# Kernel tuning notes

Measured on AMD Instinct MI355X. Metric: run time of the kernel, lower is better.

Reference implementation:

```python
import jax, jax.numpy as jnp
import numpy as np

MAX_ITERATIONS = 10
TOLERANCE = 1e-4


def setup_inputs() -> dict:
    key = jax.random.key(0)
    k1, k2 = jax.random.split(key)
    B, N = 4, 2048
    p1 = jax.random.normal(k1, (B, N, 3), dtype=jnp.float32)
    p2 = jax.random.normal(k2, (B, N, 3), dtype=jnp.float32)
    return {"p1": p1, "p2": p2}


def _get_transform(p1, p2):
    # SVD-based rigid (Kabsch) transform between matched sets p1 -> p2.
    p1c = p1.mean(-2, keepdims=True)   # [B,1,3]
    p2c = p2.mean(-2, keepdims=True)   # [B,1,3]
    q1 = p1 - p1c
    q2 = p2 - p2c
    H = jnp.einsum('bnj,bnk->bjk', q2, q1)          # p2^T @ p1, [B,3,3]
    u, s, vT = jnp.linalg.svd(H)
    v = jnp.swapaxes(vT, -1, -2)
    uT = jnp.swapaxes(u, -1, -2)
    d = jnp.linalg.det(v @ uT)                      # [B], reflection fix
    v = v.at[:, 2, 2].multiply(d)
    RT = u @ jnp.swapaxes(v, -1, -2)
    R = jnp.swapaxes(RT, -1, -2)                    # [B,3,3]
    t = p2c - p1c @ R                               # [B,1,3]
    return R, t


def _nearest_neighbor(p1, p2):
    # dist[b, j, i] = ||p2[b,j] - p1[b,i]||  (matches torch broadcast layout)
    dif = p2[:, :, None, :] - p1[:, None, :, :]     # [B,N2,N1,3]
    dist = jnp.sqrt(jnp.sum(dif * dif, axis=-1))    # [B,N2,N1]
    idx = jnp.argmin(dist, axis=-1)                 # [B,N2] (topk k=1, smallest)
    vals = jnp.take_along_axis(dist, idx[..., None], axis=-1)[..., 0]
    return vals, idx


def reference(p1, p2):
    def cond(state):
        temp_pc, it, prev_err, done = state
        return (it <= MAX_ITERATIONS) & jnp.logical_not(done)

    def body(state):
        temp_pc, it, prev_err, _ = state
        vals, idx = _nearest_neighbor(temp_pc, p2)
        mean_err = vals.mean()
        # Source indexes ori_p2 with the LAST batch's indices (nn.indices[-1])
        matched = p2[:, idx[-1], :]                 # [B,N,3]
        R, t = _get_transform(temp_pc, matched)
        new_pc = temp_pc @ R + t
        done = jnp.abs(prev_err - mean_err) < TOLERANCE
        return (new_pc, it + 1, mean_err, done)

    init = (p1, jnp.int32(0), jnp.float32(0.0), jnp.bool_(False))
    temp_pc, _, _, _ = jax.lax.while_loop(cond, body, init)

    R, t = _get_transform(p1, temp_pc)
    T = jnp.concatenate([R, jnp.swapaxes(t, 1, 2)], axis=2)  # [B,3,4]
    return T
```

## Files before the change

kernel.cpp:

```cpp
#include <hip/hip_runtime.h>

#define B 4
#define N 2048
#define MAXIT 11
#define TOL 1e-4f
#define CC 64
#define QPT 4
#define QC (256*QPT)


__device__ double det3(const double* M) {
    return M[0]*(M[4]*M[8]-M[5]*M[7])
         - M[1]*(M[3]*M[8]-M[5]*M[6])
         + M[2]*(M[3]*M[7]-M[4]*M[6]);
}

__device__ void svd3x3(const double* A, double* U, double* V, double* sig) {
    double S[9];
    for (int i = 0; i < 3; ++i)
        for (int j = 0; j < 3; ++j) {
            double s = 0.0;
            for (int k = 0; k < 3; ++k) s += A[k*3+i] * A[k*3+j];
            S[i*3+j] = s;
        }
    double Vm[9] = {1,0,0, 0,1,0, 0,0,1};
    for (int sweep = 0; sweep < 30; ++sweep) {
        double off = fabs(S[1]) + fabs(S[2]) + fabs(S[5]);
        double base = fabs(S[0]) + fabs(S[4]) + fabs(S[8]);
        if (off <= 1e-15 * base) break;
        for (int pi = 0; pi < 3; ++pi) {
            const int p = (pi == 2) ? 1 : 0;
            const int q = (pi == 0) ? 1 : 2;
            double apq = S[p*3+q];
            if (apq == 0.0) continue;
            double app = S[p*3+p], aqq = S[q*3+q];
            double tau = (aqq - app) / (2.0 * apq);
            double tt  = ((tau >= 0.0) ? 1.0 : -1.0) / (fabs(tau) + sqrt(1.0 + tau*tau));
            double c = 1.0 / sqrt(1.0 + tt*tt);
            double s = tt * c;
            for (int k = 0; k < 3; ++k) {
                double skp = S[k*3+p], skq = S[k*3+q];
                S[k*3+p] = c*skp - s*skq;
                S[k*3+q] = s*skp + c*skq;
            }
            for (int k = 0; k < 3; ++k) {
                double spk = S[p*3+k], sqk = S[q*3+k];
                S[p*3+k] = c*spk - s*sqk;
                S[q*3+k] = s*spk + c*sqk;
            }
            for (int k = 0; k < 3; ++k) {
                double vkp = Vm[k*3+p], vkq = Vm[k*3+q];
                Vm[k*3+p] = c*vkp - s*vkq;
                Vm[k*3+q] = s*vkp + c*vkq;
            }
        }
    }
    double lam[3] = {S[0], S[4], S[8]};
    int ord[3] = {0, 1, 2};
    for (int i = 0; i < 2; ++i)
        for (int j = i+1; j < 3; ++j)
            if (lam[ord[j]] > lam[ord[i]]) { int tmp = ord[i]; ord[i] = ord[j]; ord[j] = tmp; }
    for (int i = 0; i < 3; ++i) {
        int o = ord[i];
        double l = lam[o] > 0.0 ? lam[o] : 0.0;
        sig[i] = sqrt(l);
        for (int k = 0; k < 3; ++k) V[k*3+i] = Vm[k*3+o];
    }
    for (int i = 0; i < 3; ++i) {
        double u0 = 0, u1 = 0, u2 = 0;
        for (int k = 0; k < 3; ++k) {
            u0 += A[0*3+k] * V[k*3+i];
            u1 += A[1*3+k] * V[k*3+i];
            u2 += A[2*3+k] * V[k*3+i];
        }
        double nrm = sqrt(u0*u0 + u1*u1 + u2*u2);
        if (nrm > 1e-300) { u0 /= nrm; u1 /= nrm; u2 /= nrm; }
        else {
            double ax = U[0], ay = U[3], az = U[6];
            double bx = U[1], by = U[4], bz = U[7];
            u0 = ay*bz - az*by; u1 = az*bx - ax*bz; u2 = ax*by - ay*bx;
        }
        U[0*3+i] = u0; U[1*3+i] = u1; U[2*3+i] = u2;
    }
}

__device__ void compute_Rt(const double* H, const double* p1c, const double* p2c,
                           float* Rout, float* tout) {
    double U[9], V[9], sig[3];
    svd3x3(H, U, V, sig);
    double d = (det3(U) * det3(V) < 0.0) ? -1.0 : 1.0;
    V[2*3+2] *= d;
    double R[9];
    for (int i = 0; i < 3; ++i)
        for (int j = 0; j < 3; ++j) {
            double s = 0.0;
            for (int k = 0; k < 3; ++k) s += V[i*3+k] * U[j*3+k];
            R[i*3+j] = s;
        }
    for (int j = 0; j < 3; ++j) {
        double s = 0.0;
        for (int k = 0; k < 3; ++k) s += p1c[k] * R[k*3+j];
        tout[j] = (float)(p2c[j] - s);
    }
    for (int k = 0; k < 9; ++k) Rout[k] = (float)R[k];
}

__device__ inline float wred(float v) {
    v += __shfl_down(v, 32);
    v += __shfl_down(v, 16);
    v += __shfl_down(v, 8);
    v += __shfl_down(v, 4);
    v += __shfl_down(v, 2);
    v += __shfl_down(v, 1);
    return v;
}

__global__ void __launch_bounds__(256) k_init(const float* __restrict__ p1,
                                              float* __restrict__ temp,
                                              unsigned long long* __restrict__ nn0,
                                              float* scal, int* done) {
    int i = blockIdx.x * blockDim.x + threadIdx.x;
    if (i < B*N*3) temp[i] = p1[i];
    if (i < B*N)   nn0[i] = ~0ULL;
    if (i == 0)    scal[0] = 0.0f;
    if (i < 12)    done[i] = 0;
}

__global__ void __launch_bounds__(256) k_nn(const float* __restrict__ p2,
                                            const float* __restrict__ temp,
                                            unsigned long long* __restrict__ nn,
                                            const int* __restrict__ done) {
    if (*done) return;
    __shared__ float4 sc4[CC];
    const int b  = blockIdx.z;
    const int qb = blockIdx.y * QC;
    const int cb = blockIdx.x * CC;
    for (int j = threadIdx.x; j < CC; j += 256) {
        const float* cp = &temp[(b*N + cb + j)*3];
        const float cx = cp[0], cy = cp[1], cz = cp[2];
        sc4[j] = make_float4(cx, cy, cz, 0.5f*(cx*cx + cy*cy + cz*cz));
    }
    __syncthreads();

    float px[QPT], py[QPT], pz[QPT], pn[QPT];
    float best[QPT];
    int   bi[QPT];
    #pragma unroll
    for (int k = 0; k < QPT; ++k) {
        const int q = qb + threadIdx.x + 256*k;
        px[k] = p2[(b*N+q)*3+0];
        py[k] = p2[(b*N+q)*3+1];
        pz[k] = p2[(b*N+q)*3+2];
        pn[k] = px[k]*px[k] + py[k]*py[k] + pz[k]*pz[k];
        best[k] = __uint_as_float(0x7f7fffffu);
        bi[k] = 0;
    }
    #pragma unroll 4
    for (int j = 0; j < CC; ++j) {
        const float4 c = sc4[j];
        #pragma unroll
        for (int k = 0; k < QPT; ++k) {
            float s = __builtin_fmaf(-px[k], c.x,
                      __builtin_fmaf(-py[k], c.y,
                      __builtin_fmaf(-pz[k], c.z, c.w)));
            if (s < best[k]) { best[k] = s; bi[k] = cb + j; }
        }
    }
    #pragma unroll
    for (int k = 0; k < QPT; ++k) {
        const int q = qb + threadIdx.x + 256*k;
        float d2 = fmaxf(__builtin_fmaf(2.0f, best[k], pn[k]), 0.0f);
        unsigned long long pack =
            ((unsigned long long)__float_as_uint(d2) << 32) | (unsigned int)bi[k];
        atomicMin(&nn[b*N + q], pack);
    }
}

__global__ void __launch_bounds__(256) k_step(const float* __restrict__ p2,
                                              float* __restrict__ temp,
                                              const unsigned long long* __restrict__ nn_cur,
                                              unsigned long long* __restrict__ nn_next,
                                              float* scal,
                                              const int* __restrict__ done_cur,
                                              int* done_next) {
    const int t   = threadIdx.x;
    const int bid = blockIdx.x;
    if (*done_cur) {
        if (bid == 4 && t == 0) *done_next = 1;
        return;
    }

    if (bid == 4) {
        __shared__ float lds4[4];
        float s = 0.f;
        for (int i = t; i < B*N; i += 256) {
            unsigned int dbits = (unsigned int)(nn_cur[i] >> 32);
            s += sqrtf(__uint_as_float(dbits));
            nn_next[i] = ~0ULL;
        }
        s = wred(s);
        if ((t & 63) == 0) lds4[t >> 6] = s;
        __syncthreads();
        if (t == 0) {
            float tot = lds4[0] + lds4[1] + lds4[2] + lds4[3];
            float meanerr = tot / (float)(B*N);
            float prev = scal[0];
            scal[0] = meanerr;
            *done_next = (fabsf(prev - meanerr) < TOL) ? 1 : 0;
        }
        return;
    }

    const int b = bid;
    __shared__ float lred[4][9];
    __shared__ float sc1[3], sc2[3], sR[9], sT[3];
    const int wave = t >> 6, lane = t & 63;

    float v6[6] = {0,0,0,0,0,0};
    for (int i = t; i < N; i += 256) {
        const float* tp = &temp[(b*N + i)*3];
        v6[0] += tp[0]; v6[1] += tp[1]; v6[2] += tp[2];
        const int mi = (int)(unsigned int)(nn_cur[3*N + i] & 0xffffffffULL);
        const float* mp = &p2[(b*N + mi)*3];
        v6[3] += mp[0]; v6[4] += mp[1]; v6[5] += mp[2];
    }
    #pragma unroll
    for (int k = 0; k < 6; ++k) v6[k] = wred(v6[k]);
    if (lane == 0) {
        #pragma unroll
        for (int k = 0; k < 6; ++k) lred[wave][k] = v6[k];
    }
    __syncthreads();
    if (t == 0) {
        #pragma unroll
        for (int k = 0; k < 3; ++k) {
            sc1[k] = (lred[0][k]  +lred[1][k]  +lred[2][k]  +lred[3][k])   / (float)N;
            sc2[k] = (lred[0][3+k]+lred[1][3+k]+lred[2][3+k]+lred[3][3+k]) / (float)N;
        }
    }
    __syncthreads();
    const float c1x = sc1[0], c1y = sc1[1], c1z = sc1[2];
    const float c2x = sc2[0], c2y = sc2[1], c2z = sc2[2];

    float h[9];
    #pragma unroll
    for (int k = 0; k < 9; ++k) h[k] = 0.f;
    for (int i = t; i < N; i += 256) {
        const float* tp = &temp[(b*N + i)*3];
        const int mi = (int)(unsigned int)(nn_cur[3*N + i] & 0xffffffffULL);
        const float* mp = &p2[(b*N + mi)*3];
        const float bx = tp[0]-c1x, by = tp[1]-c1y, bz = tp[2]-c1z;
        const float ax = mp[0]-c2x, ay = mp[1]-c2y, az = mp[2]-c2z;
        h[0] += ax*bx; h[1] += ax*by; h[2] += ax*bz;
        h[3] += ay*bx; h[4] += ay*by; h[5] += ay*bz;
        h[6] += az*bx; h[7] += az*by; h[8] += az*bz;
    }
    #pragma unroll
    for (int k = 0; k < 9; ++k) h[k] = wred(h[k]);
    if (lane == 0) {
        #pragma unroll
        for (int k = 0; k < 9; ++k) lred[wave][k] = h[k];
    }
    __syncthreads();
    if (t == 0) {
        double H[9], c1d[3], c2d[3];
        for (int k = 0; k < 9; ++k)
            H[k] = (double)(lred[0][k]+lred[1][k]+lred[2][k]+lred[3][k]);
        c1d[0] = c1x; c1d[1] = c1y; c1d[2] = c1z;
        c2d[0] = c2x; c2d[1] = c2y; c2d[2] = c2z;
        compute_Rt(H, c1d, c2d, sR, sT);
    }
    __syncthreads();
    for (int i = t; i < N; i += 256) {
        float* tp = &temp[(b*N + i)*3];
        const float x = tp[0], y = tp[1], z = tp[2];
        tp[0] = x*sR[0] + y*sR[3] + z*sR[6] + sT[0];
        tp[1] = x*sR[1] + y*sR[4] + z*sR[7] + sT[1];
        tp[2] = x*sR[2] + y*sR[5] + z*sR[8] + sT[2];
    }
}

__global__ void __launch_bounds__(256) k_final(const float* __restrict__ p1,
                                               const float* __restrict__ temp,
                                               float* __restrict__ out) {
    const int b = blockIdx.x;
    const int t = threadIdx.x;
    __shared__ float lred[4][9];
    __shared__ float sc1[3], sc2[3], sR[9], sT[3];
    const int wave = t >> 6, lane = t & 63;

    float v6[6] = {0,0,0,0,0,0};
    for (int i = t; i < N; i += 256) {
        const float* pp = &p1[(b*N + i)*3];
        const float* tp = &temp[(b*N + i)*3];
        v6[0] += pp[0]; v6[1] += pp[1]; v6[2] += pp[2];
        v6[3] += tp[0]; v6[4] += tp[1]; v6[5] += tp[2];
    }
    #pragma unroll
    for (int k = 0; k < 6; ++k) v6[k] = wred(v6[k]);
    if (lane == 0) {
        #pragma unroll
        for (int k = 0; k < 6; ++k) lred[wave][k] = v6[k];
    }
    __syncthreads();
    if (t == 0) {
        #pragma unroll
        for (int k = 0; k < 3; ++k) {
            sc1[k] = (lred[0][k]  +lred[1][k]  +lred[2][k]  +lred[3][k])   / (float)N;
            sc2[k] = (lred[0][3+k]+lred[1][3+k]+lred[2][3+k]+lred[3][3+k]) / (float)N;
        }
    }
    __syncthreads();
    const float c1x = sc1[0], c1y = sc1[1], c1z = sc1[2];
    const float c2x = sc2[0], c2y = sc2[1], c2z = sc2[2];

    float h[9];
    #pragma unroll
    for (int k = 0; k < 9; ++k) h[k] = 0.f;
    for (int i = t; i < N; i += 256) {
        const float* pp = &p1[(b*N + i)*3];
        const float* tp = &temp[(b*N + i)*3];
        const float bx = pp[0]-c1x, by = pp[1]-c1y, bz = pp[2]-c1z;
        const float ax = tp[0]-c2x, ay = tp[1]-c2y, az = tp[2]-c2z;
        h[0] += ax*bx; h[1] += ax*by; h[2] += ax*bz;
        h[3] += ay*bx; h[4] += ay*by; h[5] += ay*bz;
        h[6] += az*bx; h[7] += az*by; h[8] += az*bz;
    }
    #pragma unroll
    for (int k = 0; k < 9; ++k) h[k] = wred(h[k]);
    if (lane == 0) {
        #pragma unroll
        for (int k = 0; k < 9; ++k) lred[wave][k] = h[k];
    }
    __syncthreads();
    if (t == 0) {
        double H[9], c1d[3], c2d[3];
        for (int k = 0; k < 9; ++k)
            H[k] = (double)(lred[0][k]+lred[1][k]+lred[2][k]+lred[3][k]);
        c1d[0] = c1x; c1d[1] = c1y; c1d[2] = c1z;
        c2d[0] = c2x; c2d[1] = c2y; c2d[2] = c2z;
        compute_Rt(H, c1d, c2d, sR, sT);
        for (int i = 0; i < 3; ++i) {
            out[b*12 + i*4 + 0] = sR[i*3+0];
            out[b*12 + i*4 + 1] = sR[i*3+1];
            out[b*12 + i*4 + 2] = sR[i*3+2];
            out[b*12 + i*4 + 3] = sT[i];
        }
    }
}

extern "C" void kernel_launch(void* const* d_in, const int* in_sizes, int n_in,
                              void* d_out, int out_size, void* d_ws, size_t ws_size,
                              hipStream_t stream) {
    const float* p1 = (const float*)d_in[0];
    const float* p2 = (const float*)d_in[1];
    float* out  = (float*)d_out;
    float* temp = (float*)d_ws;
    unsigned long long* nn0 = (unsigned long long*)((char*)d_ws + 98304);
    unsigned long long* nn1 = (unsigned long long*)((char*)d_ws + 163840);
    float* scal = (float*)((char*)d_ws + 229376);
    int*   done = (int*)((char*)d_ws + 229380);

    k_init<<<(B*N*3 + 255)/256, 256, 0, stream>>>(p1, temp, nn0, scal, done);
    dim3 g(N/CC, N/QC, B);
    for (int it = 0; it < MAXIT; ++it) {
        unsigned long long* nn_cur  = (it & 1) ? nn1 : nn0;
        unsigned long long* nn_next = (it & 1) ? nn0 : nn1;
        k_nn<<<g, 256, 0, stream>>>(p2, temp, nn_cur, &done[it]);
        k_step<<<5, 256, 0, stream>>>(p2, temp, nn_cur, nn_next, scal,
                                      &done[it], &done[it+1]);
    }
    k_final<<<4, 256, 0, stream>>>(p1, temp, out);
}
```

Measured before the change: 309.6 us.

## Fuse ICP loop into one cooperative persistent kernel with grid syncs

Replaces the roughly two dozen per-iteration kernel launches (init, NN, step, final) with one cooperative kernel of 256 blocks that uses grid.sync between phases. The transform is applied lazily to the staged points, and H is built from raw sums minus the N·c2·c1 centroid term, so one pass of per-block partial sums replaces the serial 4-block reductions. The NN buffer alternates between atomicMin and atomicMax on the complement, so it never needs a reset pass. It removes launch overhead and the serial single-block step kernels, but adds grid-wide barriers and slightly changes numerics by forming H from raw moments.

```diff
diff --git a/kernel.cpp b/kernel.cpp
--- a/kernel.cpp
+++ b/kernel.cpp
@@ -1,12 +1,18 @@
 #include <hip/hip_runtime.h>
+#include <hip/hip_cooperative_groups.h>
+
+namespace cg = cooperative_groups;
 
 #define B 4
 #define N 2048
 #define MAXIT 11
 #define TOL 1e-4f
+#define NBLK 256
+#define BT 256
 #define CC 64
 #define QPT 4
-#define QC (256*QPT)
+#define QC (BT*QPT)
+#define RPB 32
 
 
 __device__ double det3(const double* M) {
@@ -115,236 +121,235 @@
     return v;
 }
 
-__global__ void __launch_bounds__(256) k_init(const float* __restrict__ p1,
-                                              float* __restrict__ temp,
-                                              unsigned long long* __restrict__ nn0,
-                                              float* scal, int* done) {
-    int i = blockIdx.x * blockDim.x + threadIdx.x;
-    if (i < B*N*3) temp[i] = p1[i];
-    if (i < B*N)   nn0[i] = ~0ULL;
-    if (i == 0)    scal[0] = 0.0f;
-    if (i < 12)    done[i] = 0;
-}
-
-__global__ void __launch_bounds__(256) k_nn(const float* __restrict__ p2,
-                                            const float* __restrict__ temp,
-                                            unsigned long long* __restrict__ nn,
-                                            const int* __restrict__ done) {
-    if (*done) return;
+__device__ __forceinline__ void tf_pt(const float* __restrict__ R, const float* __restrict__ T,
+                                      float x, float y, float z,
+                                      float& ox, float& oy, float& oz) {
+    ox = x*R[0] + y*R[3] + z*R[6] + T[0];
+    oy = x*R[1] + y*R[4] + z*R[7] + T[1];
+    oz = x*R[2] + y*R[5] + z*R[8] + T[2];
+}
+
+__global__ void __launch_bounds__(BT, 1)
+icp_fused(const float* __restrict__ p1, const float* __restrict__ p2,
+          float* __restrict__ out, float* __restrict__ buf,
+          unsigned long long* __restrict__ nn,
+          float* __restrict__ part, float* __restrict__ p1s) {
+    cg::grid_group grid = cg::this_grid();
+    const int bid = blockIdx.x, tid = threadIdx.x;
+    const int b = bid >> 6, blk = bid & 63;
+    const int r0 = bid * RPB;
+    const int lane = tid & 63, wave = tid >> 6;
+
     __shared__ float4 sc4[CC];
-    const int b  = blockIdx.z;
-    const int qb = blockIdx.y * QC;
-    const int cb = blockIdx.x * CC;
-    for (int j = threadIdx.x; j < CC; j += 256) {
-        const float* cp = &temp[(b*N + cb + j)*3];
-        const float cx = cp[0], cy = cp[1], cz = cp[2];
-        sc4[j] = make_float4(cx, cy, cz, 0.5f*(cx*cx + cy*cy + cz*cz));
-    }
-    __syncthreads();
-
-    float px[QPT], py[QPT], pz[QPT], pn[QPT];
-    float best[QPT];
-    int   bi[QPT];
-    #pragma unroll
-    for (int k = 0; k < QPT; ++k) {
-        const int q = qb + threadIdx.x + 256*k;
-        px[k] = p2[(b*N+q)*3+0];
-        py[k] = p2[(b*N+q)*3+1];
-        pz[k] = p2[(b*N+q)*3+2];
-        pn[k] = px[k]*px[k] + py[k]*py[k] + pz[k]*pz[k];
-        best[k] = __uint_as_float(0x7f7fffffu);
-        bi[k] = 0;
-    }
-    #pragma unroll 4
-    for (int j = 0; j < CC; ++j) {
-        const float4 c = sc4[j];
+    __shared__ float sR[9], sT[3];
+    __shared__ float lred[4][3];
+    __shared__ int sCtl;
+
+    for (int j = tid; j < RPB*3; j += BT) buf[r0*3 + j] = p1[r0*3 + j];
+    if (tid < RPB) nn[r0 + tid] = ~0ULL;
+    if (blk == 0) {
+        float sx = 0.f, sy = 0.f, sz = 0.f;
+        for (int i = tid; i < N; i += BT) {
+            const float* pp = &p1[(b*N + i)*3];
+            sx += pp[0]; sy += pp[1]; sz += pp[2];
+        }
+        sx = wred(sx); sy = wred(sy); sz = wred(sz);
+        if (lane == 0) { lred[wave][0]=sx; lred[wave][1]=sy; lred[wave][2]=sz; }
+        __syncthreads();
+        if (tid == 0) {
+            p1s[b*3+0] = lred[0][0]+lred[1][0]+lred[2][0]+lred[3][0];
+            p1s[b*3+1] = lred[0][1]+lred[1][1]+lred[2][1]+lred[3][1];
+            p1s[b*3+2] = lred[0][2]+lred[1][2]+lred[2][2]+lred[3][2];
+        }
+    }
+    grid.sync();
+
+    int itex = MAXIT;
+    for (int it = 0; it <= MAXIT; ++it) {
+        if (it == 0) {
+            if (tid == 0) {
+                sR[0]=1.f; sR[1]=0.f; sR[2]=0.f;
+                sR[3]=0.f; sR[4]=1.f; sR[5]=0.f;
+                sR[6]=0.f; sR[7]=0.f; sR[8]=1.f;
+                sT[0]=0.f; sT[1]=0.f; sT[2]=0.f;
+                sCtl = 0;
+            }
+        } else if (wave == 0) {
+            const int slot  = (it-1) & 3;
+            const int slot2 = (it-2) & 3;
+            float a[16];
+            const float* pb = &part[((slot*B + b)*64 + lane)*16];
+            #pragma unroll
+            for (int k = 0; k < 16; ++k) a[k] = pb[k];
+            #pragma unroll
+            for (int k = 0; k < 16; ++k) a[k] = wred(a[k]);
+            float ec = 0.f;
+            #pragma unroll
+            for (int bb = 0; bb < B; ++bb)
+                ec += part[((slot*B + bb)*64 + lane)*16 + 15];
+            ec = wred(ec);
+            float ep = 0.f;
+            if (it >= 2) {
+                #pragma unroll
+                for (int bb = 0; bb < B; ++bb)
+                    ep += part[((slot2*B + bb)*64 + lane)*16 + 15];
+                ep = wred(ep);
+            }
+            if (lane == 0) {
+                const float errcur  = ec / (float)(B*N);
+                const float errprev = (it >= 2) ? ep / (float)(B*N) : 0.0f;
+                const int done = (fabsf(errprev - errcur) < TOL) ? 1 : 0;
+                double H[9], c1d[3], c2d[3];
+                c2d[0] = (double)a[0]/N; c2d[1] = (double)a[1]/N; c2d[2] = (double)a[2]/N;
+                c1d[0] = (double)a[3]/N; c1d[1] = (double)a[4]/N; c1d[2] = (double)a[5]/N;
+                for (int j = 0; j < 3; ++j)
+                    for (int k = 0; k < 3; ++k)
+                        H[j*3+k] = (double)a[6 + j*3 + k] - (double)N * c2d[j] * c1d[k];
+                compute_Rt(H, c1d, c2d, sR, sT);
+                sCtl = (done || it == MAXIT) ? 1 : 0;
+            }
+        }
+        __syncthreads();
+        if (sCtl) { itex = it; break; }
+
+        {
+            const int cb = (blk >> 1) * CC;
+            const int qb = (blk & 1) * QC;
+            if (tid < CC) {
+                const float* cp = &buf[(b*N + cb + tid)*3];
+                float cx, cy, cz;
+                tf_pt(sR, sT, cp[0], cp[1], cp[2], cx, cy, cz);
+                sc4[tid] = make_float4(cx, cy, cz, 0.5f*(cx*cx + cy*cy + cz*cz));
+            }
+            __syncthreads();
+            float px[QPT], py[QPT], pz[QPT];
+            float best[QPT];
+            int   bi[QPT];
+            #pragma unroll
+            for (int k = 0; k < QPT; ++k) {
+                const int q = qb + tid + BT*k;
+                px[k] = p2[(b*N + q)*3 + 0];
+                py[k] = p2[(b*N + q)*3 + 1];
+                pz[k] = p2[(b*N + q)*3 + 2];
+                best[k] = __uint_as_float(0x7f7fffffu);
+                bi[k] = 0;
+            }
+            #pragma unroll 4
+            for (int j = 0; j < CC; ++j) {
+                const float4 c = sc4[j];
+                #pragma unroll
+                for (int k = 0; k < QPT; ++k) {
+                    float s = __builtin_fmaf(-px[k], c.x,
+                              __builtin_fmaf(-py[k], c.y,
+                              __builtin_fmaf(-pz[k], c.z, c.w)));
+                    if (s < best[k]) { best[k] = s; bi[k] = cb + j; }
+                }
+            }
+            #pragma unroll
+            for (int k = 0; k < QPT; ++k) {
+                const int q = qb + tid + BT*k;
+                const float pn = px[k]*px[k] + py[k]*py[k] + pz[k]*pz[k];
+                float d2 = fmaxf(__builtin_fmaf(2.0f, best[k], pn), 0.0f);
+                unsigned long long K =
+                    ((unsigned long long)__float_as_uint(d2) << 32) | (unsigned int)bi[k];
+                if (it & 1) atomicMax(&nn[b*N + q], ~K);
+                else        atomicMin(&nn[b*N + q],  K);
+            }
+        }
+        grid.sync();
+
+        {
+            const int slotW = it & 3;
+            float pv[16];
+            #pragma unroll
+            for (int k = 0; k < 16; ++k) pv[k] = 0.f;
+            if (tid < RPB) {
+                const int r = r0 + tid;
+                const int i = r & (N-1);
+                unsigned long long pk = nn[r];
+                if (it & 1) pk = ~pk;
+                const unsigned int dbits = (unsigned int)(pk >> 32);
+                unsigned long long pk3 = nn[3*N + i];
+                if (it & 1) pk3 = ~pk3;
+                const int mi = (int)(unsigned int)(pk3 & 0xffffffffULL);
+                const float* mp = &p2[(b*N + mi)*3];
+                const float mx = mp[0], my = mp[1], mz = mp[2];
+                const float* tp = &buf[r*3];
+                float tx, ty, tz;
+                tf_pt(sR, sT, tp[0], tp[1], tp[2], tx, ty, tz);
+                buf[r*3+0] = tx; buf[r*3+1] = ty; buf[r*3+2] = tz;
+                pv[0] = mx; pv[1] = my; pv[2] = mz;
+                pv[3] = tx; pv[4] = ty; pv[5] = tz;
+                pv[6] = mx*tx;  pv[7]  = mx*ty; pv[8]  = mx*tz;
+                pv[9] = my*tx;  pv[10] = my*ty; pv[11] = my*tz;
+                pv[12]= mz*tx;  pv[13] = mz*ty; pv[14] = mz*tz;
+                pv[15]= sqrtf(__uint_as_float(dbits));
+            }
+            if (wave == 0) {
+                #pragma unroll
+                for (int k = 0; k < 16; ++k) pv[k] = wred(pv[k]);
+                if (lane == 0) {
+                    float* pb = &part[((slotW*B + b)*64 + blk)*16];
+                    #pragma unroll
+                    for (int k = 0; k < 16; ++k) pb[k] = pv[k];
+                }
+            }
+        }
+        grid.sync();
+    }
+
+    {
+        const int fslot = itex & 3;
+        float pv[12];
         #pragma unroll
-        for (int k = 0; k < QPT; ++k) {
-            float s = __builtin_fmaf(-px[k], c.x,
-                      __builtin_fmaf(-py[k], c.y,
-                      __builtin_fmaf(-pz[k], c.z, c.w)));
-            if (s < best[k]) { best[k] = s; bi[k] = cb + j; }
-        }
-    }
-    #pragma unroll
-    for (int k = 0; k < QPT; ++k) {
-        const int q = qb + threadIdx.x + 256*k;
-        float d2 = fmaxf(__builtin_fmaf(2.0f, best[k], pn[k]), 0.0f);
-        unsigned long long pack =
-            ((unsigned long long)__float_as_uint(d2) << 32) | (unsigned int)bi[k];
-        atomicMin(&nn[b*N + q], pack);
-    }
-}
-
-__global__ void __launch_bounds__(256) k_step(const float* __restrict__ p2,
-                                              float* __restrict__ temp,
-                                              const unsigned long long* __restrict__ nn_cur,
-                                              unsigned long long* __restrict__ nn_next,
-                                              float* scal,
-                                              const int* __restrict__ done_cur,
-                                              int* done_next) {
-    const int t   = threadIdx.x;
-    const int bid = blockIdx.x;
-    if (*done_cur) {
-        if (bid == 4 && t == 0) *done_next = 1;
-        return;
-    }
-
-    if (bid == 4) {
-        __shared__ float lds4[4];
-        float s = 0.f;
-        for (int i = t; i < B*N; i += 256) {
-            unsigned int dbits = (unsigned int)(nn_cur[i] >> 32);
-            s += sqrtf(__uint_as_float(dbits));
-            nn_next[i] = ~0ULL;
-        }
-        s = wred(s);
-        if ((t & 63) == 0) lds4[t >> 6] = s;
-        __syncthreads();
-        if (t == 0) {
-            float tot = lds4[0] + lds4[1] + lds4[2] + lds4[3];
-            float meanerr = tot / (float)(B*N);
-            float prev = scal[0];
-            scal[0] = meanerr;
-            *done_next = (fabsf(prev - meanerr) < TOL) ? 1 : 0;
-        }
-        return;
-    }
-
-    const int b = bid;
-    __shared__ float lred[4][9];
-    __shared__ float sc1[3], sc2[3], sR[9], sT[3];
-    const int wave = t >> 6, lane = t & 63;
-
-    float v6[6] = {0,0,0,0,0,0};
-    for (int i = t; i < N; i += 256) {
-        const float* tp = &temp[(b*N + i)*3];
-        v6[0] += tp[0]; v6[1] += tp[1]; v6[2] += tp[2];
-        const int mi = (int)(unsigned int)(nn_cur[3*N + i] & 0xffffffffULL);
-        const float* mp = &p2[(b*N + mi)*3];
-        v6[3] += mp[0]; v6[4] += mp[1]; v6[5] += mp[2];
-    }
-    #pragma unroll
-    for (int k = 0; k < 6; ++k) v6[k] = wred(v6[k]);
-    if (lane == 0) {
-        #pragma unroll
-        for (int k = 0; k < 6; ++k) lred[wave][k] = v6[k];
-    }
-    __syncthreads();
-    if (t == 0) {
-        #pragma unroll
-        for (int k = 0; k < 3; ++k) {
-            sc1[k] = (lred[0][k]  +lred[1][k]  +lred[2][k]  +lred[3][k])   / (float)N;
-            sc2[k] = (lred[0][3+k]+lred[1][3+k]+lred[2][3+k]+lred[3][3+k]) / (float)N;
-        }
-    }
-    __syncthreads();
-    const float c1x = sc1[0], c1y = sc1[1], c1z = sc1[2];
-    const float c2x = sc2[0], c2y = sc2[1], c2z = sc2[2];
-
-    float h[9];
-    #pragma unroll
-    for (int k = 0; k < 9; ++k) h[k] = 0.f;
-    for (int i = t; i < N; i += 256) {
-        const float* tp = &temp[(b*N + i)*3];
-        const int mi = (int)(unsigned int)(nn_cur[3*N + i] & 0xffffffffULL);
-        const float* mp = &p2[(b*N + mi)*3];
-        const float bx = tp[0]-c1x, by = tp[1]-c1y, bz = tp[2]-c1z;
-        const float ax = mp[0]-c2x, ay = mp[1]-c2y, az = mp[2]-c2z;
-        h[0] += ax*bx; h[1] += ax*by; h[2] += ax*bz;
-        h[3] += ay*bx; h[4] += ay*by; h[5] += ay*bz;
-        h[6] += az*bx; h[7] += az*by; h[8] += az*bz;
-    }
-    #pragma unroll
-    for (int k = 0; k < 9; ++k) h[k] = wred(h[k]);
-    if (lane == 0) {
-        #pragma unroll
-        for (int k = 0; k < 9; ++k) lred[wave][k] = h[k];
-    }
-    __syncthreads();
-    if (t == 0) {
-        double H[9], c1d[3], c2d[3];
-        for (int k = 0; k < 9; ++k)
-            H[k] = (double)(lred[0][k]+lred[1][k]+lred[2][k]+lred[3][k]);
-        c1d[0] = c1x; c1d[1] = c1y; c1d[2] = c1z;
-        c2d[0] = c2x; c2d[1] = c2y; c2d[2] = c2z;
-        compute_Rt(H, c1d, c2d, sR, sT);
-    }
-    __syncthreads();
-    for (int i = t; i < N; i += 256) {
-        float* tp = &temp[(b*N + i)*3];
-        const float x = tp[0], y = tp[1], z = tp[2];
-        tp[0] = x*sR[0] + y*sR[3] + z*sR[6] + sT[0];
-        tp[1] = x*sR[1] + y*sR[4] + z*sR[7] + sT[1];
-        tp[2] = x*sR[2] + y*sR[5] + z*sR[8] + sT[2];
-    }
-}
-
-__global__ void __launch_bounds__(256) k_final(const float* __restrict__ p1,
-                                               const float* __restrict__ temp,
-                                               float* __restrict__ out) {
-    const int b = blockIdx.x;
-    const int t = threadIdx.x;
-    __shared__ float lred[4][9];
-    __shared__ float sc1[3], sc2[3], sR[9], sT[3];
-    const int wave = t >> 6, lane = t & 63;
-
-    float v6[6] = {0,0,0,0,0,0};
-    for (int i = t; i < N; i += 256) {
-        const float* pp = &p1[(b*N + i)*3];
-        const float* tp = &temp[(b*N + i)*3];
-        v6[0] += pp[0]; v6[1] += pp[1]; v6[2] += pp[2];
-        v6[3] += tp[0]; v6[4] += tp[1]; v6[5] += tp[2];
-    }
-    #pragma unroll
-    for (int k = 0; k < 6; ++k) v6[k] = wred(v6[k]);
-    if (lane == 0) {
-        #pragma unroll
-        for (int k = 0; k < 6; ++k) lred[wave][k] = v6[k];
-    }
-    __syncthreads();
-    if (t == 0) {
-        #pragma unroll
-        for (int k = 0; k < 3; ++k) {
-            sc1[k] = (lred[0][k]  +lred[1][k]  +lred[2][k]  +lred[3][k])   / (float)N;
-            sc2[k] = (lred[0][3+k]+lred[1][3+k]+lred[2][3+k]+lred[3][3+k]) / (float)N;
-        }
-    }
-    __syncthreads();
-    const float c1x = sc1[0], c1y = sc1[1], c1z = sc1[2];
-    const float c2x = sc2[0], c2y = sc2[1], c2z = sc2[2];
-
-    float h[9];
-    #pragma unroll
-    for (int k = 0; k < 9; ++k) h[k] = 0.f;
-    for (int i = t; i < N; i += 256) {
-        const float* pp = &p1[(b*N + i)*3];
-        const float* tp = &temp[(b*N + i)*3];
-        const float bx = pp[0]-c1x, by = pp[1]-c1y, bz = pp[2]-c1z;
-        const float ax = tp[0]-c2x, ay = tp[1]-c2y, az = tp[2]-c2z;
-        h[0] += ax*bx; h[1] += ax*by; h[2] += ax*bz;
-        h[3] += ay*bx; h[4] += ay*by; h[5] += ay*bz;
-        h[6] += az*bx; h[7] += az*by; h[8] += az*bz;
-    }
-    #pragma unroll
-    for (int k = 0; k < 9; ++k) h[k] = wred(h[k]);
-    if (lane == 0) {
-        #pragma unroll
-        for (int k = 0; k < 9; ++k) lred[wave][k] = h[k];
-    }
-    __syncthreads();
-    if (t == 0) {
-        double H[9], c1d[3], c2d[3];
-        for (int k = 0; k < 9; ++k)
-            H[k] = (double)(lred[0][k]+lred[1][k]+lred[2][k]+lred[3][k]);
-        c1d[0] = c1x; c1d[1] = c1y; c1d[2] = c1z;
-        c2d[0] = c2x; c2d[1] = c2y; c2d[2] = c2z;
-        compute_Rt(H, c1d, c2d, sR, sT);
-        for (int i = 0; i < 3; ++i) {
-            out[b*12 + i*4 + 0] = sR[i*3+0];
-            out[b*12 + i*4 + 1] = sR[i*3+1];
-            out[b*12 + i*4 + 2] = sR[i*3+2];
-            out[b*12 + i*4 + 3] = sT[i];
+        for (int k = 0; k < 12; ++k) pv[k] = 0.f;
+        if (tid < RPB) {
+            const int r = r0 + tid;
+            const float* tp = &buf[r*3];
+            float tx, ty, tz;
+            tf_pt(sR, sT, tp[0], tp[1], tp[2], tx, ty, tz);
+            const float* pp = &p1[r*3];
+            const float px = pp[0], py = pp[1], pz = pp[2];
+            pv[0] = tx; pv[1] = ty; pv[2] = tz;
+            pv[3] = tx*px; pv[4] = tx*py; pv[5] = tx*pz;
+            pv[6] = ty*px; pv[7] = ty*py; pv[8] = ty*pz;
+            pv[9] = tz*px; pv[10]= tz*py; pv[11]= tz*pz;
+        }
+        if (wave == 0) {
+            #pragma unroll
+            for (int k = 0; k < 12; ++k) pv[k] = wred(pv[k]);
+            if (lane == 0) {
+                float* pb = &part[((fslot*B + b)*64 + blk)*16];
+                #pragma unroll
+                for (int k = 0; k < 12; ++k) pb[k] = pv[k];
+            }
+        }
+        grid.sync();
+        if (blk == 0 && wave == 0) {
+            float a[12];
+            const float* pb = &part[((fslot*B + b)*64 + lane)*16];
+            #pragma unroll
+            for (int k = 0; k < 12; ++k) a[k] = pb[k];
+            #pragma unroll
+            for (int k = 0; k < 12; ++k) a[k] = wred(a[k]);
+            if (lane == 0) {
+                double H[9], c1d[3], c2d[3];
+                c2d[0] = (double)a[0]/N; c2d[1] = (double)a[1]/N; c2d[2] = (double)a[2]/N;
+                c1d[0] = (double)p1s[b*3+0]/N;
+                c1d[1] = (double)p1s[b*3+1]/N;
+                c1d[2] = (double)p1s[b*3+2]/N;
+                for (int j = 0; j < 3; ++j)
+                    for (int k = 0; k < 3; ++k)
+                        H[j*3+k] = (double)a[3 + j*3 + k] - (double)N * c2d[j] * c1d[k];
+                float Rf[9], Tf[3];
+                compute_Rt(H, c1d, c2d, Rf, Tf);
+                for (int i = 0; i < 3; ++i) {
+                    out[b*12 + i*4 + 0] = Rf[i*3+0];
+                    out[b*12 + i*4 + 1] = Rf[i*3+1];
+                    out[b*12 + i*4 + 2] = Rf[i*3+2];
+                    out[b*12 + i*4 + 3] = Tf[i];
+                }
+            }
         }
     }
 }
@@ -354,21 +359,14 @@
                               hipStream_t stream) {
     const float* p1 = (const float*)d_in[0];
     const float* p2 = (const float*)d_in[1];
-    float* out  = (float*)d_out;
-    float* temp = (float*)d_ws;
-    unsigned long long* nn0 = (unsigned long long*)((char*)d_ws + 98304);
-    unsigned long long* nn1 = (unsigned long long*)((char*)d_ws + 163840);
-    float* scal = (float*)((char*)d_ws + 229376);
-    int*   done = (int*)((char*)d_ws + 229380);
-
-    k_init<<<(B*N*3 + 255)/256, 256, 0, stream>>>(p1, temp, nn0, scal, done);
-    dim3 g(N/CC, N/QC, B);
-    for (int it = 0; it < MAXIT; ++it) {
-        unsigned long long* nn_cur  = (it & 1) ? nn1 : nn0;
-        unsigned long long* nn_next = (it & 1) ? nn0 : nn1;
-        k_nn<<<g, 256, 0, stream>>>(p2, temp, nn_cur, &done[it]);
-        k_step<<<5, 256, 0, stream>>>(p2, temp, nn_cur, nn_next, scal,
-                                      &done[it], &done[it+1]);
-    }
-    k_final<<<4, 256, 0, stream>>>(p1, temp, out);
-}
+    float* out = (float*)d_out;
+    float* buf = (float*)d_ws;
+    unsigned long long* nn = (unsigned long long*)((char*)d_ws + 98304);
+    float* part = (float*)((char*)d_ws + 163840);
+    float* p1s  = (float*)((char*)d_ws + 229376);
+
+    void* args[] = { (void*)&p1, (void*)&p2, (void*)&out,
+                     (void*)&buf, (void*)&nn, (void*)&part, (void*)&p1s };
+    hipLaunchCooperativeKernel((const void*)icp_fused, dim3(NBLK), dim3(BT),
+                               args, 0, stream);
+}
```

Result: slower. 886.0 us (+186.1%).
